# Kernel optimization log

Measured on AMD Instinct MI355X. Metric: run time of the kernel, lower is better.

The kernel has to match this reference:

```python
import jax, jax.numpy as jnp
import numpy as np

WH, WW = 8, 8            # window_size
NUM_HEADS = 8
DIM = 256
CPB_HIDDEN = 512
N = WH * WW


def _make_coords_table():
    # [1, 2*WH-1, 2*WW-1, 2] log-spaced continuous relative coords (Swin-V2)
    h = np.arange(-(WH - 1), WH, dtype=np.float32)
    w = np.arange(-(WW - 1), WW, dtype=np.float32)
    gh, gw = np.meshgrid(h, w, indexing='ij')
    table = np.stack([gh, gw], axis=-1)[None]  # [1,2WH-1,2WW-1,2]
    table[..., 0] /= (WH - 1)
    table[..., 1] /= (WW - 1)
    table *= 8.0
    table = np.sign(table) * np.log2(np.abs(table) + 1.0) / np.log2(8.0)
    return jnp.asarray(table, dtype=jnp.float32)


def _make_rel_pos_index():
    ch = np.arange(WH)
    cw = np.arange(WW)
    coords = np.stack(np.meshgrid(ch, cw, indexing='ij'))   # [2,WH,WW]
    cf = coords.reshape(2, -1)                               # [2,N]
    rel = cf[:, :, None] - cf[:, None, :]                    # [2,N,N]
    rel = rel.transpose(1, 2, 0).astype(np.int32)            # [N,N,2]
    rel[..., 0] += WH - 1
    rel[..., 1] += WW - 1
    rel[..., 0] *= 2 * WW - 1
    return jnp.asarray(rel.sum(-1), dtype=jnp.int32)         # [N,N]


def setup_inputs() -> dict:
    key = jax.random.key(0)
    ks = jax.random.split(key, 8)
    B_ = 2048
    nW = 64
    x = jax.random.normal(ks[0], (B_, N, DIM), dtype=jnp.float32)
    mask = jnp.zeros((nW, N, N), dtype=jnp.float32)
    qkv_w = jax.random.normal(ks[1], (3 * DIM, DIM), dtype=jnp.float32) * 0.02
    q_bias = jnp.zeros((DIM,), dtype=jnp.float32)
    v_bias = jnp.zeros((DIM,), dtype=jnp.float32)
    logit_scale = jnp.log(10.0 * jnp.ones((NUM_HEADS, 1, 1), dtype=jnp.float32))
    cpb_w1 = jax.random.normal(ks[2], (CPB_HIDDEN, 2), dtype=jnp.float32) * 0.02
    cpb_b1 = jnp.zeros((CPB_HIDDEN,), dtype=jnp.float32)
    cpb_w2 = jax.random.normal(ks[3], (NUM_HEADS, CPB_HIDDEN), dtype=jnp.float32) * 0.02
    proj_w = jax.random.normal(ks[4], (DIM, DIM), dtype=jnp.float32) * 0.02
    proj_b = jnp.zeros((DIM,), dtype=jnp.float32)
    return {
        'x': x, 'mask': mask,
        'qkv_w': qkv_w, 'q_bias': q_bias, 'v_bias': v_bias,
        'logit_scale': logit_scale,
        'cpb_w1': cpb_w1, 'cpb_b1': cpb_b1, 'cpb_w2': cpb_w2,
        'proj_w': proj_w, 'proj_b': proj_b,
        'coords_table': _make_coords_table(),
        'rel_idx': _make_rel_pos_index(),
    }


def reference(x, mask, qkv_w, q_bias, v_bias, logit_scale,
              cpb_w1, cpb_b1, cpb_w2, proj_w, proj_b,
              coords_table, rel_idx):
    B_, n, C = x.shape
    H = NUM_HEADS
    hd = C // H

    # qkv with [q_bias, 0, v_bias]
    qkv_bias = jnp.concatenate([q_bias, jnp.zeros_like(v_bias), v_bias])
    qkv = x @ qkv_w.T + qkv_bias                         # [B,N,3C]
    qkv = qkv.reshape(B_, n, 3, H, hd).transpose(2, 0, 3, 1, 4)
    q, k, v = qkv[0], qkv[1], qkv[2]                     # [B,H,N,hd]

    # cosine attention: L2-normalized q,k (eps as in F.normalize)
    qn = q / jnp.maximum(jnp.linalg.norm(q, axis=-1, keepdims=True), 1e-12)
    kn = k / jnp.maximum(jnp.linalg.norm(k, axis=-1, keepdims=True), 1e-12)
    attn = jnp.einsum('bhnd,bhmd->bhnm', qn, kn)         # [B,H,N,N]

    max_log = jnp.log(jnp.asarray(1.0 / 0.01, dtype=x.dtype))
    scale = jnp.exp(jnp.minimum(logit_scale, max_log))   # [H,1,1]
    attn = attn * scale

    # MLP relative position bias: 2 -> 512 -> H, gather, 16*sigmoid
    hid = jax.nn.relu(coords_table @ cpb_w1.T + cpb_b1)  # [1,2WH-1,2WW-1,512]
    table = (hid @ cpb_w2.T).reshape(-1, H)              # [(2WH-1)(2WW-1), H]
    bias = table[rel_idx.reshape(-1)].reshape(n, n, H)
    bias = 16.0 * jax.nn.sigmoid(bias.transpose(2, 0, 1))  # [H,N,N]
    attn = attn + bias[None]

    nW = mask.shape[0]
    attn = attn.reshape(B_ // nW, nW, H, n, n) + mask[None, :, None]
    attn = attn.reshape(B_, H, n, n)
    attn = jax.nn.softmax(attn, axis=-1)

    out = jnp.einsum('bhnm,bhmd->bhnd', attn, v)         # [B,H,N,hd]
    out = out.transpose(0, 2, 1, 3).reshape(B_, n, C)
    return out @ proj_w.T + proj_b
```

## Files before the change

kernel.cpp:

```cpp
#include <hip/hip_runtime.h>
#include <hip/hip_bf16.h>

typedef unsigned short u16;
typedef unsigned int   u32;
typedef __attribute__((ext_vector_type(8))) short short8;
typedef __attribute__((ext_vector_type(4))) short short4v;
typedef __attribute__((ext_vector_type(4))) float f32x4;

__device__ __forceinline__ u16 f2bf(float f) {
  u32 u = __float_as_uint(f);
  u32 r = (u + 0x7fffu + ((u >> 16) & 1u)) >> 16;
  return (u16)r;
}

__global__ __launch_bounds__(256) void wcvt_kernel(
    const float* __restrict__ qkvw, const float* __restrict__ pw,
    u16* __restrict__ wq, u16* __restrict__ wp) {
  const int e = (blockIdx.x * 256 + threadIdx.x) * 4;
  if (e < 196608) {
    const float4 v = *(const float4*)(qkvw + e);
    short4v o; o[0]=(short)f2bf(v.x); o[1]=(short)f2bf(v.y);
    o[2]=(short)f2bf(v.z); o[3]=(short)f2bf(v.w);
    *(short4v*)(wq + e) = o;
  } else {
    const int e2 = e - 196608;
    const float4 v = *(const float4*)(pw + e2);
    short4v o; o[0]=(short)f2bf(v.x); o[1]=(short)f2bf(v.y);
    o[2]=(short)f2bf(v.z); o[3]=(short)f2bf(v.w);
    *(short4v*)(wp + e2) = o;
  }
}

__global__ __launch_bounds__(256) void cpb_kernel(
    const float* __restrict__ ct, const float* __restrict__ w1,
    const float* __restrict__ b1, const float* __restrict__ w2,
    float* __restrict__ table) {
  const int r = blockIdx.x;
  const int t = threadIdx.x;
  const int lane = t & 63, wave = t >> 6;
  const float c0 = ct[r * 2 + 0];
  const float c1 = ct[r * 2 + 1];
  float acc[8] = {0.f, 0.f, 0.f, 0.f, 0.f, 0.f, 0.f, 0.f};
  for (int j = t; j < 512; j += 256) {
    float hid = fmaxf(c0 * w1[j * 2] + c1 * w1[j * 2 + 1] + b1[j], 0.f);
#pragma unroll
    for (int hh = 0; hh < 8; ++hh) acc[hh] += hid * w2[hh * 512 + j];
  }
#pragma unroll
  for (int hh = 0; hh < 8; ++hh)
#pragma unroll
    for (int off = 1; off < 64; off <<= 1) acc[hh] += __shfl_xor(acc[hh], off);
  __shared__ float red[4][8];
  if (lane == 0)
#pragma unroll
    for (int hh = 0; hh < 8; ++hh) red[wave][hh] = acc[hh];
  __syncthreads();
  if (t < 8) table[r * 8 + t] = red[0][t] + red[1][t] + red[2][t] + red[3][t];
}

__global__ __launch_bounds__(256) void bm_kernel(
    const float* __restrict__ table, const int* __restrict__ rel,
    const float* __restrict__ mask, float* __restrict__ bmP) {
  const int g = blockIdx.x * 256 + threadIdx.x;
  const int w = g >> 13;
  const int h = (g >> 10) & 7;
  const int m = (g >> 4) & 63;
  const int l = g & 15;
  float4 o;
#pragma unroll
  for (int j = 0; j < 4; ++j) {
    const int c = j * 16 + l;
    const float t = table[rel[m * 64 + c] * 8 + h];
    o[j] = 16.f / (1.f + __expf(-t)) + mask[(size_t)w * 4096 + m * 64 + c];
  }
  *(float4*)(bmP + ((((size_t)w * 8 + h) * 64 + m) * 64 + l * 4)) = o;
}

__global__ __launch_bounds__(512, 2) void fused_kernel(
    const float* __restrict__ X,
    const float* __restrict__ bmP,
    const float* __restrict__ lsc,
    const u16*  __restrict__ Wqb,
    const float* __restrict__ qb, const float* __restrict__ vbias,
    const u16*  __restrict__ Wpb,
    const float* __restrict__ pb,
    float* __restrict__ out) {
  __shared__ __attribute__((aligned(16))) u16 sA[16896];
  __shared__ __attribute__((aligned(16))) u16 sB[36864];
  __shared__ __attribute__((aligned(16))) u16 sV[18432];

  const int bw = blockIdx.x;
  const int w  = bw & 63;
  const int tid  = threadIdx.x;
  const int wave = tid >> 6, lane = tid & 63;
  const int l15 = lane & 15, l4 = lane >> 4;

  {
    const int cq  = tid & 7;
    const int rlo = tid >> 3;
    const float* xrow = X + ((size_t)bw * 64 + rlo) * 256;
#pragma unroll
    for (int kf = 0; kf < 8; ++kf) {
      const float4 xv = *(const float4*)(xrow + kf * 32 + cq * 4);
      short4v t4; t4[0]=(short)f2bf(xv.x); t4[1]=(short)f2bf(xv.y);
      t4[2]=(short)f2bf(xv.z); t4[3]=(short)f2bf(xv.w);
      *(short4v*)&sA[kf * 2048 + rlo * 32 + cq * 4] = t4;
    }
  }
  __syncthreads();

  {
    const u16* wbase = Wqb + (size_t)(wave * 96 + l15) * 256 + l4 * 8;
    f32x4 acc[4][6];
#pragma unroll
    for (int mi = 0; mi < 4; ++mi)
#pragma unroll
      for (int nj = 0; nj < 6; ++nj) acc[mi][nj] = (f32x4){0.f, 0.f, 0.f, 0.f};

    short8 bf_cur[6];
#pragma unroll
    for (int nj = 0; nj < 6; ++nj)
      bf_cur[nj] = *(const short8*)(wbase + (size_t)(nj * 16) * 256);

#pragma unroll
    for (int kf = 0; kf < 8; ++kf) {
      short8 af[4];
#pragma unroll
      for (int mi = 0; mi < 4; ++mi)
        af[mi] = *(const short8*)&sA[kf * 2048 + (mi * 16 + l15) * 32 + l4 * 8];
      short8 bf_nxt[6];
      if (kf < 7) {
#pragma unroll
        for (int nj = 0; nj < 6; ++nj)
          bf_nxt[nj] = *(const short8*)(wbase + (size_t)(nj * 16) * 256 + (kf + 1) * 32);
      }
#pragma unroll
      for (int nj = 0; nj < 6; ++nj)
#pragma unroll
        for (int mi = 0; mi < 4; ++mi)
          acc[mi][nj] = __builtin_amdgcn_mfma_f32_16x16x32_bf16(af[mi], bf_cur[nj], acc[mi][nj], 0, 0, 0);
      if (kf < 7) {
#pragma unroll
        for (int nj = 0; nj < 6; ++nj) bf_cur[nj] = bf_nxt[nj];
      }
    }

#pragma unroll
    for (int t = 0; t < 3; ++t) {
      const int nbase = wave * 96 + t * 32;
      const int which = nbase >> 8;
      const int h = (nbase >> 5) & 7;
      const int c = nbase & 255;
      if (which <= 1) {
        u16* dst = (which == 0 ? sB : sB + 16384) + h * 2048;
        const float b0 = (which == 0) ? qb[c + l15] : 0.f;
        const float b1 = (which == 0) ? qb[c + 16 + l15] : 0.f;
#pragma unroll
        for (int mi = 0; mi < 4; ++mi)
#pragma unroll
          for (int r = 0; r < 4; ++r) {
            const float v0 = acc[mi][2 * t][r] + b0;
            const float v1 = acc[mi][2 * t + 1][r] + b1;
            float ss = v0 * v0 + v1 * v1;
            ss += __shfl_xor(ss, 1); ss += __shfl_xor(ss, 2);
            ss += __shfl_xor(ss, 4); ss += __shfl_xor(ss, 8);
            const float inv = 1.f / fmaxf(sqrtf(ss), 1e-12f);
            const int m = mi * 16 + l4 * 4 + r;
            dst[m * 32 + l15]      = f2bf(v0 * inv);
            dst[m * 32 + 16 + l15] = f2bf(v1 * inv);
          }
      } else {
        const float b0 = vbias[c + l15];
        const float b1 = vbias[c + 16 + l15];
        u16* dst = sV + h * 2304;
#pragma unroll
        for (int mi = 0; mi < 4; ++mi)
#pragma unroll
          for (int r = 0; r < 4; ++r) {
            const int m = mi * 16 + l4 * 4 + r;
            dst[l15 * 72 + m]        = f2bf(acc[mi][2 * t][r] + b0);
            dst[(16 + l15) * 72 + m] = f2bf(acc[mi][2 * t + 1][r] + b1);
          }
      }
    }
  }
  __syncthreads();

  {
    const int h = wave;
    const float* bmbase = bmP + (((size_t)(w * 8 + h)) * 64) * 64 + l15 * 4;
    float4 bmv[4][4];
#pragma unroll
    for (int i = 0; i < 4; ++i)
#pragma unroll
      for (int r = 0; r < 4; ++r) {
        const int m = i * 16 + l4 * 4 + r;
        bmv[i][r] = *(const float4*)(bmbase + (size_t)m * 64);
      }

    short8 aq[4], bk[4];
#pragma unroll
    for (int i = 0; i < 4; ++i)
      aq[i] = *(const short8*)&sB[h * 2048 + (i * 16 + l15) * 32 + l4 * 8];
#pragma unroll
    for (int j = 0; j < 4; ++j)
      bk[j] = *(const short8*)&sB[16384 + h * 2048 + (j * 16 + l15) * 32 + l4 * 8];

    f32x4 s[4][4];
#pragma unroll
    for (int i = 0; i < 4; ++i)
#pragma unroll
      for (int j = 0; j < 4; ++j) {
        const f32x4 z = {0.f, 0.f, 0.f, 0.f};
        s[i][j] = __builtin_amdgcn_mfma_f32_16x16x32_bf16(aq[i], bk[j], z, 0, 0, 0);
      }
    __syncthreads();

    const float scale = expf(fminf(lsc[h], 4.60517018598809136804f));
    u16* pW = sB + wave * 4608;

#pragma unroll
    for (int i = 0; i < 4; ++i)
#pragma unroll
      for (int r = 0; r < 4; ++r) {
        const int m = i * 16 + l4 * 4 + r;
        float v0[4]; float mx = -3.0e38f;
#pragma unroll
        for (int j = 0; j < 4; ++j) {
          const float sv = s[i][j][r] * scale + bmv[i][r][j];
          v0[j] = sv; mx = fmaxf(mx, sv);
        }
        mx = fmaxf(mx, __shfl_xor(mx, 1)); mx = fmaxf(mx, __shfl_xor(mx, 2));
        mx = fmaxf(mx, __shfl_xor(mx, 4)); mx = fmaxf(mx, __shfl_xor(mx, 8));
        float sum = 0.f;
#pragma unroll
        for (int j = 0; j < 4; ++j) { v0[j] = __expf(v0[j] - mx); sum += v0[j]; }
        sum += __shfl_xor(sum, 1); sum += __shfl_xor(sum, 2);
        sum += __shfl_xor(sum, 4); sum += __shfl_xor(sum, 8);
        const float isum = 1.f / sum;
#pragma unroll
        for (int j = 0; j < 4; ++j)
          pW[m * 72 + j * 16 + l15] = f2bf(v0[j] * isum);
      }

    f32x4 oa[4][2];
#pragma unroll
    for (int i = 0; i < 4; ++i)
#pragma unroll
      for (int nb = 0; nb < 2; ++nb) oa[i][nb] = (f32x4){0.f, 0.f, 0.f, 0.f};
#pragma unroll
    for (int kb = 0; kb < 2; ++kb) {
      short8 pa[4];
#pragma unroll
      for (int i = 0; i < 4; ++i)
        pa[i] = *(const short8*)&pW[(i * 16 + l15) * 72 + kb * 32 + l4 * 8];
#pragma unroll
      for (int nb = 0; nb < 2; ++nb) {
        const short8 vb8 = *(const short8*)&sV[h * 2304 + (nb * 16 + l15) * 72 + kb * 32 + l4 * 8];
#pragma unroll
        for (int i = 0; i < 4; ++i)
          oa[i][nb] = __builtin_amdgcn_mfma_f32_16x16x32_bf16(pa[i], vb8, oa[i][nb], 0, 0, 0);
      }
    }
#pragma unroll
    for (int i = 0; i < 4; ++i)
#pragma unroll
      for (int nb = 0; nb < 2; ++nb)
#pragma unroll
        for (int r = 0; r < 4; ++r) {
          const int m = i * 16 + l4 * 4 + r;
          sA[m * 264 + h * 32 + nb * 16 + l15] = f2bf(oa[i][nb][r]);
        }
  }
  __syncthreads();

  {
    const int n0 = wave * 32;
    const u16* pbase = Wpb + (size_t)(n0 + l15) * 256 + l4 * 8;
    f32x4 pacc[4][2];
#pragma unroll
    for (int mi = 0; mi < 4; ++mi)
#pragma unroll
      for (int nj = 0; nj < 2; ++nj) pacc[mi][nj] = (f32x4){0.f, 0.f, 0.f, 0.f};

    short8 bfr_cur[2];
#pragma unroll
    for (int nj = 0; nj < 2; ++nj)
      bfr_cur[nj] = *(const short8*)(pbase + (size_t)(nj * 16) * 256);

#pragma unroll
    for (int ks = 0; ks < 8; ++ks) {
      const int k0 = ks * 32;
      short8 afr[4];
#pragma unroll
      for (int mi = 0; mi < 4; ++mi)
        afr[mi] = *(const short8*)&sA[(mi * 16 + l15) * 264 + k0 + l4 * 8];
      short8 bfr_nxt[2];
      if (ks < 7) {
#pragma unroll
        for (int nj = 0; nj < 2; ++nj)
          bfr_nxt[nj] = *(const short8*)(pbase + (size_t)(nj * 16) * 256 + k0 + 32);
      }
#pragma unroll
      for (int nj = 0; nj < 2; ++nj)
#pragma unroll
        for (int mi = 0; mi < 4; ++mi)
          pacc[mi][nj] = __builtin_amdgcn_mfma_f32_16x16x32_bf16(afr[mi], bfr_cur[nj], pacc[mi][nj], 0, 0, 0);
      if (ks < 7) {
#pragma unroll
        for (int nj = 0; nj < 2; ++nj) bfr_cur[nj] = bfr_nxt[nj];
      }
    }
    float* orow = out + (size_t)bw * 64 * 256;
#pragma unroll
    for (int mi = 0; mi < 4; ++mi)
#pragma unroll
      for (int nj = 0; nj < 2; ++nj) {
        const int n = n0 + nj * 16 + l15;
        const float bias = pb[n];
#pragma unroll
        for (int r = 0; r < 4; ++r) {
          const int m = mi * 16 + l4 * 4 + r;
          orow[(size_t)m * 256 + n] = pacc[mi][nj][r] + bias;
        }
      }
  }
}

extern "C" void kernel_launch(void* const* d_in, const int* in_sizes, int n_in,
                              void* d_out, int out_size, void* d_ws, size_t ws_size,
                              hipStream_t stream) {
  (void)in_sizes; (void)n_in; (void)out_size; (void)ws_size;
  const float* x    = (const float*)d_in[0];
  const float* mask = (const float*)d_in[1];
  const float* qkvw = (const float*)d_in[2];
  const float* qb   = (const float*)d_in[3];
  const float* vb   = (const float*)d_in[4];
  const float* lsc  = (const float*)d_in[5];
  const float* w1   = (const float*)d_in[6];
  const float* b1   = (const float*)d_in[7];
  const float* w2   = (const float*)d_in[8];
  const float* pw   = (const float*)d_in[9];
  const float* pb   = (const float*)d_in[10];
  const float* ct   = (const float*)d_in[11];
  const int* rel    = (const int*)d_in[12];
  float* out = (float*)d_out;

  char* ws = (char*)d_ws;
  float* table = (float*)(ws);
  u16* Wqb = (u16*)(ws + 262144);
  u16* Wpb = (u16*)(ws + 720896);
  float* bmP = (float*)(ws + (1 << 20));

  wcvt_kernel<<<256, 256, 0, stream>>>(qkvw, pw, Wqb, Wpb);
  cpb_kernel<<<225, 256, 0, stream>>>(ct, w1, b1, w2, table);
  bm_kernel<<<2048, 256, 0, stream>>>(table, rel, mask, bmP);
  fused_kernel<<<2048, 512, 0, stream>>>(x, bmP, lsc, Wqb, qb, vb,
                                         Wpb, pb, out);
}
```

Measured before the change: 498.6 us.

## Assign per-head QKV columns to each wave to drop cross-wave LDS exchange

Each wave now computes the Q, K and V projection columns for its own head instead of an arbitrary 96-column slice. Normalized q/k and transposed v are staged in a per-wave LDS region, so attention can start without a block-wide barrier between the QKV projection and attention. One barrier is removed, the separate sB/sV buffers are merged into per-wave buffers, and s_setprio hints are wrapped around the MFMA bursts. The weight loads now touch three strided row groups per wave, and an extra barrier is added before the attention output is written into sA, which shares storage with the X tile.

```diff
diff --git a/kernel.cpp b/kernel.cpp
--- a/kernel.cpp
+++ b/kernel.cpp
@@ -86,14 +86,14 @@
     const float* __restrict__ pb,
     float* __restrict__ out) {
   __shared__ __attribute__((aligned(16))) u16 sA[16896];
-  __shared__ __attribute__((aligned(16))) u16 sB[36864];
-  __shared__ __attribute__((aligned(16))) u16 sV[18432];
+  __shared__ __attribute__((aligned(16))) u16 sW[8][6912];
 
   const int bw = blockIdx.x;
   const int w  = bw & 63;
   const int tid  = threadIdx.x;
   const int wave = tid >> 6, lane = tid & 63;
   const int l15 = lane & 15, l4 = lane >> 4;
+  const int h = wave;
 
   {
     const int cq  = tid & 7;
@@ -109,8 +109,14 @@
   }
   __syncthreads();
 
+  u16* vt   = &sW[wave][0];
+  u16* pbuf = &sW[wave][2304];
+
+  f32x4 oa[4][2];
+
   {
-    const u16* wbase = Wqb + (size_t)(wave * 96 + l15) * 256 + l4 * 8;
+    const int rb[6] = {h * 32, h * 32 + 16, 256 + h * 32, 256 + h * 32 + 16,
+                       512 + h * 32, 512 + h * 32 + 16};
     f32x4 acc[4][6];
 #pragma unroll
     for (int mi = 0; mi < 4; ++mi)
@@ -120,7 +126,7 @@
     short8 bf_cur[6];
 #pragma unroll
     for (int nj = 0; nj < 6; ++nj)
-      bf_cur[nj] = *(const short8*)(wbase + (size_t)(nj * 16) * 256);
+      bf_cur[nj] = *(const short8*)(Wqb + (size_t)(rb[nj] + l15) * 256 + l4 * 8);
 
 #pragma unroll
     for (int kf = 0; kf < 8; ++kf) {
@@ -132,7 +138,7 @@
       if (kf < 7) {
 #pragma unroll
         for (int nj = 0; nj < 6; ++nj)
-          bf_nxt[nj] = *(const short8*)(wbase + (size_t)(nj * 16) * 256 + (kf + 1) * 32);
+          bf_nxt[nj] = *(const short8*)(Wqb + (size_t)(rb[nj] + l15) * 256 + (kf + 1) * 32 + l4 * 8);
       }
 #pragma unroll
       for (int nj = 0; nj < 6; ++nj)
@@ -145,49 +151,51 @@
       }
     }
 
-#pragma unroll
-    for (int t = 0; t < 3; ++t) {
-      const int nbase = wave * 96 + t * 32;
-      const int which = nbase >> 8;
-      const int h = (nbase >> 5) & 7;
-      const int c = nbase & 255;
-      if (which <= 1) {
-        u16* dst = (which == 0 ? sB : sB + 16384) + h * 2048;
-        const float b0 = (which == 0) ? qb[c + l15] : 0.f;
-        const float b1 = (which == 0) ? qb[c + 16 + l15] : 0.f;
-#pragma unroll
-        for (int mi = 0; mi < 4; ++mi)
-#pragma unroll
-          for (int r = 0; r < 4; ++r) {
-            const float v0 = acc[mi][2 * t][r] + b0;
-            const float v1 = acc[mi][2 * t + 1][r] + b1;
-            float ss = v0 * v0 + v1 * v1;
-            ss += __shfl_xor(ss, 1); ss += __shfl_xor(ss, 2);
-            ss += __shfl_xor(ss, 4); ss += __shfl_xor(ss, 8);
-            const float inv = 1.f / fmaxf(sqrtf(ss), 1e-12f);
-            const int m = mi * 16 + l4 * 4 + r;
-            dst[m * 32 + l15]      = f2bf(v0 * inv);
-            dst[m * 32 + 16 + l15] = f2bf(v1 * inv);
-          }
-      } else {
-        const float b0 = vbias[c + l15];
-        const float b1 = vbias[c + 16 + l15];
-        u16* dst = sV + h * 2304;
-#pragma unroll
-        for (int mi = 0; mi < 4; ++mi)
-#pragma unroll
-          for (int r = 0; r < 4; ++r) {
-            const int m = mi * 16 + l4 * 4 + r;
-            dst[l15 * 72 + m]        = f2bf(acc[mi][2 * t][r] + b0);
-            dst[(16 + l15) * 72 + m] = f2bf(acc[mi][2 * t + 1][r] + b1);
-          }
-      }
-    }
-  }
-  __syncthreads();
-
-  {
-    const int h = wave;
+    u16* qstage = pbuf;
+    u16* kstage = pbuf + 2048;
+    {
+      const float qb0 = qb[h * 32 + l15];
+      const float qb1 = qb[h * 32 + 16 + l15];
+#pragma unroll
+      for (int mi = 0; mi < 4; ++mi)
+#pragma unroll
+        for (int r = 0; r < 4; ++r) {
+          const float v0 = acc[mi][0][r] + qb0;
+          const float v1 = acc[mi][1][r] + qb1;
+          float ss = v0 * v0 + v1 * v1;
+          ss += __shfl_xor(ss, 1); ss += __shfl_xor(ss, 2);
+          ss += __shfl_xor(ss, 4); ss += __shfl_xor(ss, 8);
+          const float inv = 1.f / fmaxf(sqrtf(ss), 1e-12f);
+          const int m = mi * 16 + l4 * 4 + r;
+          qstage[m * 32 + l15]      = f2bf(v0 * inv);
+          qstage[m * 32 + 16 + l15] = f2bf(v1 * inv);
+        }
+#pragma unroll
+      for (int mi = 0; mi < 4; ++mi)
+#pragma unroll
+        for (int r = 0; r < 4; ++r) {
+          const float v0 = acc[mi][2][r];
+          const float v1 = acc[mi][3][r];
+          float ss = v0 * v0 + v1 * v1;
+          ss += __shfl_xor(ss, 1); ss += __shfl_xor(ss, 2);
+          ss += __shfl_xor(ss, 4); ss += __shfl_xor(ss, 8);
+          const float inv = 1.f / fmaxf(sqrtf(ss), 1e-12f);
+          const int m = mi * 16 + l4 * 4 + r;
+          kstage[m * 32 + l15]      = f2bf(v0 * inv);
+          kstage[m * 32 + 16 + l15] = f2bf(v1 * inv);
+        }
+      const float vb0 = vbias[h * 32 + l15];
+      const float vb1 = vbias[h * 32 + 16 + l15];
+#pragma unroll
+      for (int mi = 0; mi < 4; ++mi)
+#pragma unroll
+        for (int r = 0; r < 4; ++r) {
+          const int m = mi * 16 + l4 * 4 + r;
+          vt[l15 * 72 + m]        = f2bf(acc[mi][4][r] + vb0);
+          vt[(16 + l15) * 72 + m] = f2bf(acc[mi][5][r] + vb1);
+        }
+    }
+
     const float* bmbase = bmP + (((size_t)(w * 8 + h)) * 64) * 64 + l15 * 4;
     float4 bmv[4][4];
 #pragma unroll
@@ -201,12 +209,13 @@
     short8 aq[4], bk[4];
 #pragma unroll
     for (int i = 0; i < 4; ++i)
-      aq[i] = *(const short8*)&sB[h * 2048 + (i * 16 + l15) * 32 + l4 * 8];
+      aq[i] = *(const short8*)&qstage[(i * 16 + l15) * 32 + l4 * 8];
 #pragma unroll
     for (int j = 0; j < 4; ++j)
-      bk[j] = *(const short8*)&sB[16384 + h * 2048 + (j * 16 + l15) * 32 + l4 * 8];
+      bk[j] = *(const short8*)&kstage[(j * 16 + l15) * 32 + l4 * 8];
 
     f32x4 s[4][4];
+    __builtin_amdgcn_s_setprio(1);
 #pragma unroll
     for (int i = 0; i < 4; ++i)
 #pragma unroll
@@ -214,10 +223,10 @@
         const f32x4 z = {0.f, 0.f, 0.f, 0.f};
         s[i][j] = __builtin_amdgcn_mfma_f32_16x16x32_bf16(aq[i], bk[j], z, 0, 0, 0);
       }
-    __syncthreads();
-
-    const float scale = expf(fminf(lsc[h], 4.60517018598809136804f));
-    u16* pW = sB + wave * 4608;
+    __builtin_amdgcn_s_setprio(0);
+
+    const float scale = __expf(fminf(lsc[h], 4.60517018598809136804f));
+    u16* pW = pbuf;
 
 #pragma unroll
     for (int i = 0; i < 4; ++i)
@@ -243,7 +252,6 @@
           pW[m * 72 + j * 16 + l15] = f2bf(v0[j] * isum);
       }
 
-    f32x4 oa[4][2];
 #pragma unroll
     for (int i = 0; i < 4; ++i)
 #pragma unroll
@@ -254,24 +262,29 @@
 #pragma unroll
       for (int i = 0; i < 4; ++i)
         pa[i] = *(const short8*)&pW[(i * 16 + l15) * 72 + kb * 32 + l4 * 8];
+      __builtin_amdgcn_s_setprio(1);
 #pragma unroll
       for (int nb = 0; nb < 2; ++nb) {
-        const short8 vb8 = *(const short8*)&sV[h * 2304 + (nb * 16 + l15) * 72 + kb * 32 + l4 * 8];
+        const short8 vb8 = *(const short8*)&vt[(nb * 16 + l15) * 72 + kb * 32 + l4 * 8];
 #pragma unroll
         for (int i = 0; i < 4; ++i)
           oa[i][nb] = __builtin_amdgcn_mfma_f32_16x16x32_bf16(pa[i], vb8, oa[i][nb], 0, 0, 0);
       }
-    }
-#pragma unroll
-    for (int i = 0; i < 4; ++i)
-#pragma unroll
-      for (int nb = 0; nb < 2; ++nb)
-#pragma unroll
-        for (int r = 0; r < 4; ++r) {
-          const int m = i * 16 + l4 * 4 + r;
-          sA[m * 264 + h * 32 + nb * 16 + l15] = f2bf(oa[i][nb][r]);
-        }
-  }
+      __builtin_amdgcn_s_setprio(0);
+    }
+  }
+
+  __syncthreads();
+
+#pragma unroll
+  for (int i = 0; i < 4; ++i)
+#pragma unroll
+    for (int nb = 0; nb < 2; ++nb)
+#pragma unroll
+      for (int r = 0; r < 4; ++r) {
+        const int m = i * 16 + l4 * 4 + r;
+        sA[m * 264 + h * 32 + nb * 16 + l15] = f2bf(oa[i][nb][r]);
+      }
   __syncthreads();
 
   {
```

After: 472.9 us. 1.05x faster.
